# Optimization experiments

Measured on AMD Instinct MI355X. Metric: run time of the kernel, lower is better.

## Reference

```python
import jax, jax.numpy as jnp
import numpy as np

DENSE_W = 0.7  # unused in learned fusion path but kept for parity
SPARSE_W = 0.3

def _l2norm(x):
    return x / jnp.linalg.norm(x, axis=-1, keepdims=True)

def setup_inputs() -> dict:
    key = jax.random.key(0)
    ks = jax.random.split(key, 8)
    Q, D, dim = 32, 4096, 384
    feat = 2 * dim + 2  # 770
    query_dense = _l2norm(jax.random.normal(ks[0], (Q, dim), jnp.float32))
    doc_dense = _l2norm(jax.random.normal(ks[1], (D, dim), jnp.float32))
    sparse_scores = jax.random.uniform(ks[2], (Q, D), jnp.float32)
    W1 = jax.random.normal(ks[3], (feat, 384), jnp.float32) * (1.0 / np.sqrt(feat))
    b1 = jnp.zeros((384,), jnp.float32)
    W2 = jax.random.normal(ks[4], (384, 192), jnp.float32) * (1.0 / np.sqrt(384))
    b2 = jnp.zeros((192,), jnp.float32)
    W3 = jax.random.normal(ks[5], (192, 1), jnp.float32) * (1.0 / np.sqrt(192))
    b3 = jnp.zeros((1,), jnp.float32)
    return {"query_dense": query_dense, "doc_dense": doc_dense,
            "sparse_scores": sparse_scores,
            "W1": W1, "b1": b1, "W2": W2, "b2": b2, "W3": W3, "b3": b3}

def reference(query_dense, doc_dense, sparse_scores, W1, b1, W2, b2, W3, b3):
    # dense cosine similarity (inputs are L2-normalized): [Q, D]
    dense_scores = query_dense @ doc_dense.T
    Q, D = dense_scores.shape
    dim = query_dense.shape[1]
    # Vectorized equivalent of the per-pair gather+concat double loop:
    # feature[q, d] = [query_dense[q], doc_dense[d], dense[q,d], sparse[q,d]]
    qf = jnp.broadcast_to(query_dense[:, None, :], (Q, D, dim))
    df = jnp.broadcast_to(doc_dense[None, :, :], (Q, D, dim))
    features = jnp.concatenate(
        [qf, df, dense_scores[..., None], sparse_scores[..., None]], axis=-1)  # [Q, D, 2*dim+2]
    # 4-layer fusion MLP (Dropout is identity at inference)
    h = jax.nn.relu(features @ W1 + b1)
    h = jax.nn.relu(h @ W2 + b2)
    fusion_weights = jax.nn.sigmoid((h @ W3 + b3)[..., 0])  # [Q, D]
    final_scores = fusion_weights * dense_scores + (1.0 - fusion_weights) * sparse_scores
    return final_scores, dense_scores, sparse_scores
```

## Files before the change

kernel.cpp:

```cpp
#include <hip/hip_runtime.h>
#include <hip/hip_bf16.h>

typedef __attribute__((ext_vector_type(2)))  float f32x2;
typedef __attribute__((ext_vector_type(4)))  float f32x4;
typedef __attribute__((ext_vector_type(16))) float f32x16;
typedef __attribute__((ext_vector_type(8)))  short bf16x8;
typedef __attribute__((ext_vector_type(2)))  unsigned int u32x2;
typedef __attribute__((ext_vector_type(4)))  unsigned int u32x4;

__device__ __forceinline__ short f2bf(float x){
    __hip_bfloat16 h = __float2bfloat16(x);
    return __builtin_bit_cast(short, h);
}
__device__ __forceinline__ float bf2f(short x){
    unsigned int u = ((unsigned int)(unsigned short)x) << 16;
    return __builtin_bit_cast(float, u);
}
__device__ __forceinline__ unsigned int cvt2(float lo, float hi){
    unsigned int r;
    asm("v_cvt_pk_bf16_f32 %0, %1, %2" : "=v"(r) : "v"(lo), "v"(hi));
    return r;
}

__global__ __launch_bounds__(256)
void pre0_kernel(const float* __restrict__ query, const float* __restrict__ doc,
                 const float* __restrict__ sparse, const float* __restrict__ W1,
                 const float* __restrict__ W2,
                 float* __restrict__ out_dense, float* __restrict__ out_sparse,
                 short* __restrict__ W1t, short* __restrict__ docb, short* __restrict__ qb16,
                 float* __restrict__ W1cdf, short* __restrict__ W2t){
    __shared__ float ldsq[32*388];
    __shared__ float ldsd[16*388];
    const int b = blockIdx.x, tid = threadIdx.x;

    if (b < 256){
        const int d0 = b*16;
        #pragma unroll
        for (int i=0;i<12;i++){ int idx = tid + i*256; int row = idx/96, c4 = idx%96;
            *(f32x4*)(ldsq + row*388 + c4*4) = *(const f32x4*)(query + row*384 + c4*4); }
        #pragma unroll
        for (int i=0;i<6;i++){ int idx = tid + i*256; int row = idx/96, c4 = idx%96;
            *(f32x4*)(ldsd + row*388 + c4*4) = *(const f32x4*)(doc + (d0+row)*384 + c4*4); }
        __syncthreads();
        const int q = tid>>3, dg = tid&7;
        const f32x4* q4  = (const f32x4*)(ldsq + q*388);
        const f32x4* d4a = (const f32x4*)(ldsd + dg*388);
        const f32x4* d4b = (const f32x4*)(ldsd + (dg+8)*388);
        f32x4 s0 = {0.f,0.f,0.f,0.f}, s1 = {0.f,0.f,0.f,0.f};
        #pragma unroll 4
        for (int k=0;k<96;k++){
            const f32x4 qv = q4[k];
            s0 += qv*d4a[k];
            s1 += qv*d4b[k];
        }
        out_dense[q*4096 + d0 + dg]     = s0[0]+s0[1]+s0[2]+s0[3];
        out_dense[q*4096 + d0 + dg + 8] = s1[0]+s1[1]+s1[2]+s1[3];
        if (tid < 128){
            int qq = tid>>2, c4 = tid&3;
            *(f32x4*)(out_sparse + qq*4096 + d0 + c4*4) = *(const f32x4*)(sparse + qq*4096 + d0 + c4*4);
        }
    } else if (b < 328){
        const int lt0 = (b-256)*256 + tid;
        #pragma unroll
        for (int i=0;i<2;i++){
            const int lt    = lt0 + i*18432;
            const int chunk = lt >> 6, lane = lt & 63;
            const int cl = lane & 15, quad = lane >> 4;
            const int half = (chunk >= 288) ? 1 : 0;
            const int cs = chunk - half*288;
            const int s = cs/24, ct = cs%24;
            const float* src = W1 + (half*384 + s*32 + quad*8)*384 + ct*16 + cl;
            float v[8];
            #pragma unroll
            for (int j=0;j<8;j++) v[j] = src[j*384];
            u32x4 o;
            o[0] = cvt2(v[0],v[1]); o[1] = cvt2(v[2],v[3]);
            o[2] = cvt2(v[4],v[5]); o[3] = cvt2(v[6],v[7]);
            *(u32x4*)(W1t + chunk*512 + lane*8) = o;
        }
    } else if (b < 424){
        const int t0 = (b-328)*256 + tid;
        #pragma unroll
        for (int i=0;i<16;i++){
            const int g = t0 + i*24576;
            const f32x4 v = *(const f32x4*)(doc + g*4);
            u32x2 o; o[0] = cvt2(v[0],v[1]); o[1] = cvt2(v[2],v[3]);
            *(u32x2*)(docb + g*4) = o;
        }
    } else if (b == 424){
        #pragma unroll
        for (int i=0;i<12;i++){
            const int g = tid + i*256;
            const f32x4 v = *(const f32x4*)(query + g*4);
            u32x2 o; o[0] = cvt2(v[0],v[1]); o[1] = cvt2(v[2],v[3]);
            *(u32x2*)(qb16 + g*4) = o;
        }
    } else if (b == 425){
        #pragma unroll
        for (int i=0;i<3;i++){
            int o = tid + i*256;
            W1cdf[o] = (o < 384) ? W1[768*384 + o] : W1[769*384 + (o - 384)];
        }
    } else {
        const int t0 = (b - 426)*256 + tid;
        #pragma unroll
        for (int i=0;i<9;i++){
            int c = t0 + i*1024;
            int lane_c = c & 63, st = c >> 6;
            int s = st/12, t2 = st%12;
            int n = t2*16 + (lane_c&15), kb = s*32 + ((lane_c>>4)&3)*8;
            bf16x8 v;
            #pragma unroll
            for (int j=0;j<8;j++) v[j] = f2bf(W2[(kb+j)*192 + n]);
            *(bf16x8*)(W2t + c*8) = v;
        }
    }
}

__global__ __launch_bounds__(256)
void pre1_kernel(const short* __restrict__ docb, const short* __restrict__ qb16,
                 const short* __restrict__ W1t, const float* __restrict__ b1,
                 short* __restrict__ Bws, float* __restrict__ Aq){
    const int b = blockIdx.x, tid = threadIdx.x;
    const int w = tid >> 6, lane = tid & 63;
    const int cl = lane & 15, quad = lane >> 4;

    const short* src; const short* wt; int r0; bool isA;
    if (b < 256){ r0 = b*16;       src = docb; wt = W1t + 147456; isA = false; }
    else        { r0 = (b-256)*16; src = qb16; wt = W1t;          isA = true;  }

    const short* ap = src + (r0+cl)*384 + quad*8;
    const short* wp = wt + (w*6)*512 + lane*8;

    f32x4 acc[6];
    #pragma unroll
    for (int t=0;t<6;t++) acc[t] = (f32x4){0.f,0.f,0.f,0.f};

    bf16x8 a_c = *(const bf16x8*)(ap);
    bf16x8 b_c[6];
    #pragma unroll
    for (int tt=0;tt<6;tt++) b_c[tt] = *(const bf16x8*)(wp + tt*512);

    #pragma unroll 1
    for (int s=0;s<12;s++){
        const int sn = (s < 11) ? s+1 : 0;
        const bf16x8 a_n = *(const bf16x8*)(ap + sn*32);
        bf16x8 b_n[6];
        #pragma unroll
        for (int tt=0;tt<6;tt++) b_n[tt] = *(const bf16x8*)(wp + sn*12288 + tt*512);
        #pragma unroll
        for (int tt=0;tt<6;tt++)
            acc[tt] = __builtin_amdgcn_mfma_f32_16x16x32_bf16(a_c, b_c[tt], acc[tt], 0, 0, 0);
        a_c = a_n;
        #pragma unroll
        for (int tt=0;tt<6;tt++) b_c[tt] = b_n[tt];
    }

    #pragma unroll
    for (int tt=0;tt<6;tt++){
        const int col = (w*6+tt)*16 + cl;
        if (isA){
            const float b1v = b1[col];
            #pragma unroll
            for (int r=0;r<4;r++)
                Aq[(r0 + quad*4 + r)*384 + col] = acc[tt][r] + b1v;
        } else {
            #pragma unroll
            for (int r=0;r<4;r++)
                Bws[(r0 + quad*4 + r)*384 + col] = f2bf(acc[tt][r]);
        }
    }
}

__global__ __launch_bounds__(1024)
void main_kernel(const float* __restrict__ Aq, const short* __restrict__ Bws,
                 const float* __restrict__ W1cdf, const short* __restrict__ W2t,
                 const float* __restrict__ b2, const float* __restrict__ W3,
                 const float* __restrict__ b3, const float* __restrict__ sparse,
                 const float* __restrict__ dense_in, float* __restrict__ out_final){
    __shared__ __align__(16) short lw[73728];
    __shared__ __align__(16) float lcd[768];
    const int tid = threadIdx.x;

    #pragma unroll
    for (int i=0;i<9;i++){
        int c = tid + i*1024;
        *(f32x4*)(lw + c*8) = *(const f32x4*)(W2t + c*8);
    }
    if (tid < 192)
        *(f32x4*)(lcd + tid*4) = *(const f32x4*)(W1cdf + tid*4);
    __syncthreads();

    const int lane = tid & 63, w = tid >> 6;
    const int colslot = w >> 1, mhalf = w & 1;
    const int cl = lane & 15, g = lane >> 4;
    const int mrow = mhalf*16 + cl;
    const int k8 = g*8;
    const float b3v = b3[0];
    const int dcol0 = blockIdx.x*16 + colslot;

    #pragma unroll 1
    for (int t4=0; t4<2; t4++){
        const int dcol = dcol0 + t4*8;
        const float dsv = dense_in[mrow*4096 + dcol];
        const float ssv = sparse[mrow*4096 + dcol];
        const f32x2 dsv2 = {dsv, dsv}, ssv2 = {ssv, ssv};

        f32x4 acc[12];
        #pragma unroll
        for (int t=0;t<12;t++) acc[t] = (f32x4){0.f,0.f,0.f,0.f};

        const short* bp = Bws + dcol*384;
        const float* ap = Aq + mrow*384;

        bf16x8 bwC = *(const bf16x8*)(bp + k8);
        f32x4  aC0 = *(const f32x4*)(ap + k8);
        f32x4  aC1 = *(const f32x4*)(ap + k8 + 4);

        #pragma unroll 1
        for (int s=0; s<12; s++){
            const int kn = (s < 11) ? (s+1)*32 + k8 : k8;
            const bf16x8 bwN = *(const bf16x8*)(bp + kn);
            const f32x4  aN0 = *(const f32x4*)(ap + kn);
            const f32x4  aN1 = *(const f32x4*)(ap + kn + 4);

            const int kf = s*32 + k8;
            const f32x4 wcA = *(const f32x4*)(lcd + kf);
            const f32x4 wcB = *(const f32x4*)(lcd + kf + 4);
            const f32x4 wdA = *(const f32x4*)(lcd + 384 + kf);
            const f32x4 wdB = *(const f32x4*)(lcd + 384 + kf + 4);

            u32x4 frw;
            { f32x2 h = {aC0[0] + bf2f(bwC[0]), aC0[1] + bf2f(bwC[1])};
              h += dsv2 * (f32x2){wcA[0],wcA[1]}; h += ssv2 * (f32x2){wdA[0],wdA[1]};
              frw[0] = cvt2(fmaxf(h[0],0.f), fmaxf(h[1],0.f)); }
            { f32x2 h = {aC0[2] + bf2f(bwC[2]), aC0[3] + bf2f(bwC[3])};
              h += dsv2 * (f32x2){wcA[2],wcA[3]}; h += ssv2 * (f32x2){wdA[2],wdA[3]};
              frw[1] = cvt2(fmaxf(h[0],0.f), fmaxf(h[1],0.f)); }
            { f32x2 h = {aC1[0] + bf2f(bwC[4]), aC1[1] + bf2f(bwC[5])};
              h += dsv2 * (f32x2){wcB[0],wcB[1]}; h += ssv2 * (f32x2){wdB[0],wdB[1]};
              frw[2] = cvt2(fmaxf(h[0],0.f), fmaxf(h[1],0.f)); }
            { f32x2 h = {aC1[2] + bf2f(bwC[6]), aC1[3] + bf2f(bwC[7])};
              h += dsv2 * (f32x2){wcB[2],wcB[3]}; h += ssv2 * (f32x2){wdB[2],wdB[3]};
              frw[3] = cvt2(fmaxf(h[0],0.f), fmaxf(h[1],0.f)); }
            const bf16x8 fr = __builtin_bit_cast(bf16x8, frw);

            const short* lp = lw + s*6144 + lane*8;
            #pragma unroll
            for (int tg=0; tg<4; tg++){
                const bf16x8 f0 = *(const bf16x8*)(lp + (tg*3+0)*512);
                const bf16x8 f1 = *(const bf16x8*)(lp + (tg*3+1)*512);
                const bf16x8 f2 = *(const bf16x8*)(lp + (tg*3+2)*512);
                acc[tg*3+0] = __builtin_amdgcn_mfma_f32_16x16x32_bf16(fr, f0, acc[tg*3+0], 0, 0, 0);
                acc[tg*3+1] = __builtin_amdgcn_mfma_f32_16x16x32_bf16(fr, f1, acc[tg*3+1], 0, 0, 0);
                acc[tg*3+2] = __builtin_amdgcn_mfma_f32_16x16x32_bf16(fr, f2, acc[tg*3+2], 0, 0, 0);
            }
            bwC = bwN; aC0 = aN0; aC1 = aN1;
        }

        float p0=0.f, p1=0.f, p2=0.f, p3=0.f;
        #pragma unroll
        for (int t=0;t<12;t++){
            const int n = t*16 + cl;
            const float b2v = b2[n];
            const float w3v = W3[n];
            p0 += fmaxf(acc[t][0] + b2v, 0.0f) * w3v;
            p1 += fmaxf(acc[t][1] + b2v, 0.0f) * w3v;
            p2 += fmaxf(acc[t][2] + b2v, 0.0f) * w3v;
            p3 += fmaxf(acc[t][3] + b2v, 0.0f) * w3v;
        }
        #pragma unroll
        for (int mask=1; mask<16; mask<<=1){
            p0 += __shfl_xor(p0, mask);
            p1 += __shfl_xor(p1, mask);
            p2 += __shfl_xor(p2, mask);
            p3 += __shfl_xor(p3, mask);
        }
        float myp = p0;
        myp = (cl==1) ? p1 : myp;
        myp = (cl==2) ? p2 : myp;
        myp = (cl==3) ? p3 : myp;
        if (cl < 4){
            const int row = mhalf*16 + g*4 + cl;
            const float logit = myp + b3v;
            const float wgt = 1.0f/(1.0f + __expf(-logit));
            const float dd = dense_in[row*4096 + dcol];
            const float ss = sparse[row*4096 + dcol];
            out_final[row*4096 + dcol] = wgt*dd + (1.0f - wgt)*ss;
        }
    }
}

extern "C" void kernel_launch(void* const* d_in, const int* in_sizes, int n_in,
                              void* d_out, int out_size, void* d_ws, size_t ws_size,
                              hipStream_t stream){
    const float* query  = (const float*)d_in[0];
    const float* doc    = (const float*)d_in[1];
    const float* sparse = (const float*)d_in[2];
    const float* W1     = (const float*)d_in[3];
    const float* b1     = (const float*)d_in[4];
    const float* W2     = (const float*)d_in[5];
    const float* b2     = (const float*)d_in[6];
    const float* W3     = (const float*)d_in[7];
    const float* b3     = (const float*)d_in[8];

    float* out_final  = (float*)d_out;
    float* out_dense  = (float*)d_out + 131072;
    float* out_sparse = (float*)d_out + 262144;

    short* Bws   = (short*)d_ws;
    float* Aq    = (float*)((char*)d_ws + 3145728);
    float* W1cdf = (float*)((char*)d_ws + 3194880);
    short* W2t   = (short*)((char*)d_ws + 3197952);
    short* W1t   = (short*)((char*)d_ws + 3345408);
    short* docb  = (short*)((char*)d_ws + 3935232);
    short* qb16  = (short*)((char*)d_ws + 7080960);

    hipLaunchKernelGGL(pre0_kernel, dim3(430), dim3(256), 0, stream,
                       query, doc, sparse, W1, W2, out_dense, out_sparse,
                       W1t, docb, qb16, W1cdf, W2t);
    hipLaunchKernelGGL(pre1_kernel, dim3(258), dim3(256), 0, stream,
                       docb, qb16, W1t, b1, Bws, Aq);
    hipLaunchKernelGGL(main_kernel, dim3(256), dim3(1024), 0, stream,
                       Aq, Bws, W1cdf, W2t, b2, W3, b3, sparse, out_dense, out_final);
}
```

Baseline: 125.3 us.

## Compute dense cosine scores via bf16 MFMA inside the W1 projection kernel

Removes the fp32 LDS-based dot-product blocks from the preprocessing kernel. Dense scores are instead computed in pre1 with an extra bf16 MFMA per k-step that reuses the already-loaded doc fragments against the bf16 query. The sparse passthrough copy also moves into pre1. This shrinks pre0's grid and avoids re-reading doc in fp32, at the cost of bf16 precision for the dense_scores output and a bit more work per pre1 block.

```diff
diff --git a/kernel.cpp b/kernel.cpp
--- a/kernel.cpp
+++ b/kernel.cpp
@@ -3,7 +3,6 @@
 
 typedef __attribute__((ext_vector_type(2)))  float f32x2;
 typedef __attribute__((ext_vector_type(4)))  float f32x4;
-typedef __attribute__((ext_vector_type(16))) float f32x16;
 typedef __attribute__((ext_vector_type(8)))  short bf16x8;
 typedef __attribute__((ext_vector_type(2)))  unsigned int u32x2;
 typedef __attribute__((ext_vector_type(4)))  unsigned int u32x4;
@@ -24,43 +23,13 @@
 
 __global__ __launch_bounds__(256)
 void pre0_kernel(const float* __restrict__ query, const float* __restrict__ doc,
-                 const float* __restrict__ sparse, const float* __restrict__ W1,
-                 const float* __restrict__ W2,
-                 float* __restrict__ out_dense, float* __restrict__ out_sparse,
+                 const float* __restrict__ W1, const float* __restrict__ W2,
                  short* __restrict__ W1t, short* __restrict__ docb, short* __restrict__ qb16,
                  float* __restrict__ W1cdf, short* __restrict__ W2t){
-    __shared__ float ldsq[32*388];
-    __shared__ float ldsd[16*388];
     const int b = blockIdx.x, tid = threadIdx.x;
 
-    if (b < 256){
-        const int d0 = b*16;
-        #pragma unroll
-        for (int i=0;i<12;i++){ int idx = tid + i*256; int row = idx/96, c4 = idx%96;
-            *(f32x4*)(ldsq + row*388 + c4*4) = *(const f32x4*)(query + row*384 + c4*4); }
-        #pragma unroll
-        for (int i=0;i<6;i++){ int idx = tid + i*256; int row = idx/96, c4 = idx%96;
-            *(f32x4*)(ldsd + row*388 + c4*4) = *(const f32x4*)(doc + (d0+row)*384 + c4*4); }
-        __syncthreads();
-        const int q = tid>>3, dg = tid&7;
-        const f32x4* q4  = (const f32x4*)(ldsq + q*388);
-        const f32x4* d4a = (const f32x4*)(ldsd + dg*388);
-        const f32x4* d4b = (const f32x4*)(ldsd + (dg+8)*388);
-        f32x4 s0 = {0.f,0.f,0.f,0.f}, s1 = {0.f,0.f,0.f,0.f};
-        #pragma unroll 4
-        for (int k=0;k<96;k++){
-            const f32x4 qv = q4[k];
-            s0 += qv*d4a[k];
-            s1 += qv*d4b[k];
-        }
-        out_dense[q*4096 + d0 + dg]     = s0[0]+s0[1]+s0[2]+s0[3];
-        out_dense[q*4096 + d0 + dg + 8] = s1[0]+s1[1]+s1[2]+s1[3];
-        if (tid < 128){
-            int qq = tid>>2, c4 = tid&3;
-            *(f32x4*)(out_sparse + qq*4096 + d0 + c4*4) = *(const f32x4*)(sparse + qq*4096 + d0 + c4*4);
-        }
-    } else if (b < 328){
-        const int lt0 = (b-256)*256 + tid;
+    if (b < 72){
+        const int lt0 = b*256 + tid;
         #pragma unroll
         for (int i=0;i<2;i++){
             const int lt    = lt0 + i*18432;
@@ -78,8 +47,8 @@
             o[2] = cvt2(v[4],v[5]); o[3] = cvt2(v[6],v[7]);
             *(u32x4*)(W1t + chunk*512 + lane*8) = o;
         }
-    } else if (b < 424){
-        const int t0 = (b-328)*256 + tid;
+    } else if (b < 168){
+        const int t0 = (b-72)*256 + tid;
         #pragma unroll
         for (int i=0;i<16;i++){
             const int g = t0 + i*24576;
@@ -87,7 +56,7 @@
             u32x2 o; o[0] = cvt2(v[0],v[1]); o[1] = cvt2(v[2],v[3]);
             *(u32x2*)(docb + g*4) = o;
         }
-    } else if (b == 424){
+    } else if (b == 168){
         #pragma unroll
         for (int i=0;i<12;i++){
             const int g = tid + i*256;
@@ -95,14 +64,14 @@
             u32x2 o; o[0] = cvt2(v[0],v[1]); o[1] = cvt2(v[2],v[3]);
             *(u32x2*)(qb16 + g*4) = o;
         }
-    } else if (b == 425){
+    } else if (b == 169){
         #pragma unroll
         for (int i=0;i<3;i++){
             int o = tid + i*256;
             W1cdf[o] = (o < 384) ? W1[768*384 + o] : W1[769*384 + (o - 384)];
         }
     } else {
-        const int t0 = (b - 426)*256 + tid;
+        const int t0 = (b - 170)*256 + tid;
         #pragma unroll
         for (int i=0;i<9;i++){
             int c = t0 + i*1024;
@@ -120,7 +89,9 @@
 __global__ __launch_bounds__(256)
 void pre1_kernel(const short* __restrict__ docb, const short* __restrict__ qb16,
                  const short* __restrict__ W1t, const float* __restrict__ b1,
-                 short* __restrict__ Bws, float* __restrict__ Aq){
+                 const float* __restrict__ sparse,
+                 short* __restrict__ Bws, float* __restrict__ Aq,
+                 float* __restrict__ out_dense, float* __restrict__ out_sparse){
     const int b = blockIdx.x, tid = threadIdx.x;
     const int w = tid >> 6, lane = tid & 63;
     const int cl = lane & 15, quad = lane >> 4;
@@ -129,14 +100,18 @@
     if (b < 256){ r0 = b*16;       src = docb; wt = W1t + 147456; isA = false; }
     else        { r0 = (b-256)*16; src = qb16; wt = W1t;          isA = true;  }
 
+    const int tq = w & 1;
     const short* ap = src + (r0+cl)*384 + quad*8;
     const short* wp = wt + (w*6)*512 + lane*8;
+    const short* qp = qb16 + (tq*16 + cl)*384 + quad*8;
 
     f32x4 acc[6];
     #pragma unroll
     for (int t=0;t<6;t++) acc[t] = (f32x4){0.f,0.f,0.f,0.f};
+    f32x4 accd = (f32x4){0.f,0.f,0.f,0.f};
 
     bf16x8 a_c = *(const bf16x8*)(ap);
+    bf16x8 qd_c = *(const bf16x8*)(qp);
     bf16x8 b_c[6];
     #pragma unroll
     for (int tt=0;tt<6;tt++) b_c[tt] = *(const bf16x8*)(wp + tt*512);
@@ -144,14 +119,16 @@
     #pragma unroll 1
     for (int s=0;s<12;s++){
         const int sn = (s < 11) ? s+1 : 0;
-        const bf16x8 a_n = *(const bf16x8*)(ap + sn*32);
+        const bf16x8 a_n  = *(const bf16x8*)(ap + sn*32);
+        const bf16x8 qd_n = *(const bf16x8*)(qp + sn*32);
         bf16x8 b_n[6];
         #pragma unroll
         for (int tt=0;tt<6;tt++) b_n[tt] = *(const bf16x8*)(wp + sn*12288 + tt*512);
         #pragma unroll
         for (int tt=0;tt<6;tt++)
             acc[tt] = __builtin_amdgcn_mfma_f32_16x16x32_bf16(a_c, b_c[tt], acc[tt], 0, 0, 0);
-        a_c = a_n;
+        accd = __builtin_amdgcn_mfma_f32_16x16x32_bf16(a_c, qd_c, accd, 0, 0, 0);
+        a_c = a_n; qd_c = qd_n;
         #pragma unroll
         for (int tt=0;tt<6;tt++) b_c[tt] = b_n[tt];
     }
@@ -168,6 +145,18 @@
             #pragma unroll
             for (int r=0;r<4;r++)
                 Bws[(r0 + quad*4 + r)*384 + col] = f2bf(acc[tt][r]);
+        }
+    }
+    if (!isA){
+        if (w < 2){
+            #pragma unroll
+            for (int r=0;r<4;r++)
+                out_dense[(tq*16 + cl)*4096 + r0 + quad*4 + r] = accd[r];
+        }
+        if (tid < 128){
+            const int qq = tid>>2, c4 = tid&3;
+            *(f32x4*)(out_sparse + qq*4096 + r0 + c4*4) =
+                *(const f32x4*)(sparse + qq*4096 + r0 + c4*4);
         }
     }
 }
@@ -316,11 +305,10 @@
     short* docb  = (short*)((char*)d_ws + 3935232);
     short* qb16  = (short*)((char*)d_ws + 7080960);
 
-    hipLaunchKernelGGL(pre0_kernel, dim3(430), dim3(256), 0, stream,
-                       query, doc, sparse, W1, W2, out_dense, out_sparse,
-                       W1t, docb, qb16, W1cdf, W2t);
+    hipLaunchKernelGGL(pre0_kernel, dim3(174), dim3(256), 0, stream,
+                       query, doc, W1, W2, W1t, docb, qb16, W1cdf, W2t);
     hipLaunchKernelGGL(pre1_kernel, dim3(258), dim3(256), 0, stream,
-                       docb, qb16, W1t, b1, Bws, Aq);
+                       docb, qb16, W1t, b1, sparse, Bws, Aq, out_dense, out_sparse);
     hipLaunchKernelGGL(main_kernel, dim3(256), dim3(1024), 0, stream,
                        Aq, Bws, W1cdf, W2t, b2, W3, b3, sparse, out_dense, out_final);
 }
```

Measured after the change: 123.4 us. About the same (-1.5%).
